# Optimization experiments

Hardware: AMD Instinct MI355X
Metric: run time of the kernel (lower is better)

The kernel has to match this reference:

```python
import jax, jax.numpy as jnp
import numpy as np

B, NPER, K = 32, 256, 32
N, E = B * NPER, B * NPER * 32
H, NF, NG, L = 128, 128, 50, 6
CUTOFF = 10.0
LOG2 = 0.6931471805599453


def _ssp(x):
    # ShiftedSoftplus: softplus(x) - log(2)
    return jax.nn.softplus(x) - LOG2


def setup_inputs() -> dict:
    key = jax.random.key(0)
    ks = jax.random.split(key, 16)
    rng = np.random.default_rng(0)

    pos = jnp.asarray(rng.uniform(0.0, 5.0, size=(N, 3)).astype(np.float32))
    z = jnp.asarray(rng.integers(1, 100, size=(N,)).astype(np.int32))
    batch = jnp.asarray((np.arange(N) // NPER).astype(np.int32))
    # K neighbors per atom, within the same graph, no self-loops; dst sorted
    dst = np.repeat(np.arange(N), K)
    off = rng.integers(1, NPER, size=N * K)
    src = (dst % NPER + off) % NPER + (dst // NPER) * NPER
    edge_index = jnp.asarray(np.stack([src, dst]).astype(np.int32))
    domain_ids = jnp.asarray(rng.integers(0, 5, size=(B,)).astype(np.int32))

    def dense(k, i, o):
        return jax.random.normal(k, (i, o), jnp.float32) / np.sqrt(i)

    def stackw(k, i, o):
        return jax.random.normal(k, (L, i, o), jnp.float32) / np.sqrt(i)

    return {
        'pos': pos, 'z': z, 'batch': batch, 'edge_index': edge_index,
        'domain_ids': domain_ids,
        'embedding': jax.random.normal(ks[0], (100, H), jnp.float32),
        'mlp_w1': stackw(ks[1], NG, NF), 'mlp_b1': jnp.zeros((L, NF), jnp.float32),
        'mlp_w2': stackw(ks[2], NF, NF), 'mlp_b2': jnp.zeros((L, NF), jnp.float32),
        'cf_lin1_w': stackw(ks[3], H, NF),
        'cf_lin2_w': stackw(ks[4], NF, H), 'cf_lin2_b': jnp.zeros((L, H), jnp.float32),
        'int_lin_w': stackw(ks[5], H, H), 'int_lin_b': jnp.zeros((L, H), jnp.float32),
        'out_w1': dense(ks[6], H, H // 2), 'out_b1': jnp.zeros((H // 2,), jnp.float32),
        'out_w2': dense(ks[7], H // 2, 1), 'out_b2': jnp.zeros((1,), jnp.float32),
        'dom_emb': jax.random.normal(ks[8], (5, 64), jnp.float32),
        'film_w1': dense(ks[9], 64, 128), 'film_b1': jnp.zeros((128,), jnp.float32),
        'film_w2': dense(ks[10], 128, 128), 'film_b2': jnp.zeros((128,), jnp.float32),
        'gamma_w': dense(ks[11], 128, H), 'gamma_b': jnp.zeros((H,), jnp.float32),
        'beta_w': dense(ks[12], 128, H), 'beta_b': jnp.zeros((H,), jnp.float32),
    }


def reference(pos, z, batch, edge_index, domain_ids, embedding,
              mlp_w1, mlp_b1, mlp_w2, mlp_b2, cf_lin1_w, cf_lin2_w, cf_lin2_b,
              int_lin_w, int_lin_b, out_w1, out_b1, out_w2, out_b2,
              dom_emb, film_w1, film_b1, film_w2, film_b2,
              gamma_w, gamma_b, beta_w, beta_b):
    n_atoms = pos.shape[0]
    n_graphs = domain_ids.shape[0]
    src, dst = edge_index[0], edge_index[1]

    # edge distances, gaussian smearing, cosine cutoff (computed once)
    d = jnp.sqrt(jnp.sum((pos[src] - pos[dst]) ** 2, axis=-1))          # [E]
    offsets = jnp.linspace(0.0, CUTOFF, NG).astype(pos.dtype)
    coeff = -0.5 / (CUTOFF / (NG - 1)) ** 2
    edge_attr = jnp.exp(coeff * (d[:, None] - offsets) ** 2)            # [E,NG]
    C = 0.5 * (jnp.cos(d * (np.pi / CUTOFF)) + 1.0)                     # [E]

    h = embedding[z]                                                    # [N,H]
    for l in range(L):
        # filter network on gaussian basis, modulated by cosine cutoff
        W = (_ssp(edge_attr @ mlp_w1[l] + mlp_b1[l]) @ mlp_w2[l] + mlp_b2[l]) * C[:, None]  # [E,NF]
        x = h @ cf_lin1_w[l]                                            # [N,NF]
        msg = x[src] * W                                                # [E,NF]
        agg = jax.ops.segment_sum(msg, dst, num_segments=n_atoms)       # [N,NF]
        x = agg @ cf_lin2_w[l] + cf_lin2_b[l]                           # [N,H]
        h = h + _ssp(x) @ int_lin_w[l] + int_lin_b[l]                   # residual

    atom_e = _ssp(h @ out_w1 + out_b1) @ out_w2 + out_b2                # [N,1]
    e_graph = jax.ops.segment_sum(atom_e, batch, num_segments=n_graphs) # [B,1]

    # FiLM domain bias (features are zeros, so gamma path contributes 0 - faithful)
    de = dom_emb[domain_ids]                                            # [B,64]
    film = jax.nn.relu(de @ film_w1 + film_b1) @ film_w2 + film_b2      # [B,128]
    gamma = film @ gamma_w + gamma_b                                    # [B,H]
    beta = film @ beta_w + beta_b                                       # [B,H]
    dummy = jnp.zeros((n_graphs, H), pos.dtype)
    bias = jnp.sum(gamma * dummy + beta, axis=-1)                       # [B]

    # faithful broadcast [B,1]+[B] -> [B,B], then sum(dim=1) as in original
    energy = jnp.sum(e_graph + bias[None, :], axis=1)                   # [B]

    forces = jnp.zeros((n_atoms, 3), energy.dtype)
    stress = jnp.zeros((n_graphs, 3, 3), energy.dtype)
    features = jnp.zeros((n_atoms, H), energy.dtype)
    return energy, forces, stress, features
```

## Files before the change

kernel.cpp:

```cpp
#include <hip/hip_runtime.h>
#include <math.h>

using uint = unsigned int;
typedef _Float16 h2    __attribute__((ext_vector_type(2)));
typedef _Float16 f16x8 __attribute__((ext_vector_type(8)));
typedef float    f32x4 __attribute__((ext_vector_type(4)));

#define N_ATOMS 8192
#define NEDGE   262144
#define KNBR    32
#define NGAUSS  50
#define NLAYER  6
#define NB      32
#define GTAB    1024
#define DMAX    8.6603f
#define FCUT    10.0f
#define MB      1048576

#define LSTRIDE 76
#define S_WT    0
#define S_AS    9728
#define S_TS    10944
#define GEMM_SMEM 12160

#define T_W1    0
#define T_W2    4096
#define T_RBF   12288
#define T_HID   13312
#define TAB_SMEM 15360

#define OW1P_OFF 147456
#define M1_OFF   151552
#define M2_OFF   176128
#define WPACK_N  225280

__device__ __forceinline__ float ssp(float x) {
    return fmaxf(x, 0.0f) + log1pf(expf(-fabsf(x))) - 0.69314718055994531f;
}
__device__ __forceinline__ uint pack2(float a, float b) {
    union { h2 h; uint u; } x;
    h2 v; v.x = (_Float16)a; v.y = (_Float16)b; x.h = v; return x.u;
}
__device__ __forceinline__ h2 u2h(uint u) {
    union { uint u; h2 h; } x; x.u = u; return x.h;
}
__device__ __forceinline__ uint h2u(h2 h) {
    union { h2 h; uint u; } x; x.h = h; return x.u;
}
__device__ __forceinline__ float fdot2f(h2 a, h2 b, float c) {
#if __has_builtin(__builtin_amdgcn_fdot2)
    return __builtin_amdgcn_fdot2(a, b, c, false);
#else
    return fmaf((float)a.y, (float)b.y, fmaf((float)a.x, (float)b.x, c));
#endif
}

__device__ __forceinline__ void stage_cp(uint* sm, const uint* __restrict__ src,
                                         int n16, int tid) {
    for (int i = tid; i < n16; i += 256) {
        uint4 v = ((const uint4*)src)[i];
        *(uint4*)&sm[(i >> 4) * LSTRIDE + (i & 15) * 4] = v;
    }
}

template<int NCT>
__device__ __forceinline__ void run_gemm(const uint* sm, int as_off, int lane,
                                         int nb, f32x4* acc) {
    int m = lane & 15, q = lane >> 4;
    #pragma unroll
    for (int ks = 0; ks < 4; ++ks) {
        f16x8 a = *(const f16x8*)&sm[as_off + m * LSTRIDE + q * 4 + ks * 16];
        #pragma unroll
        for (int ct = 0; ct < NCT; ++ct) {
            f16x8 b = *(const f16x8*)&sm[S_WT + (nb + ct * 16 + m) * LSTRIDE + q * 4 + ks * 16];
            acc[ct] = __builtin_amdgcn_mfma_f32_16x16x32_f16(a, b, acc[ct], 0, 0, 0);
        }
    }
}

struct SArgs {
    const float *pos; const int *z; const int *ei; const int *dom;
    const float *emb;
    const float *cf1; const float *cf2w; const float *intw; const float *ow1;
    const float *mw1; const float *mw2;
    const float *dome; const float *fw1; const float *fb1;
    const float *fw2; const float *fb2; const float *bw; const float *bb;
    uint2 *epack; float *h; uint *xA;
    float *gbias; uint *wpack; float *out; int out_size;
};

__global__ void __launch_bounds__(256) k_setup(SArgs a) {
    __shared__ __align__(16) uint sm[S_AS + 1216];
    const int tid = threadIdx.x, bid = blockIdx.x;
    const int gidx = bid * 256 + tid, gsz = 512 * 256;
    const int lane = tid & 63, w = tid >> 6;
    const int m = lane & 15, q = lane >> 4;
    const int rowbase = bid * 16;

    for (int i = gidx; i < a.out_size; i += gsz) a.out[i] = 0.0f;

    for (int idx = gidx; idx < WPACK_N; idx += gsz) {
        if (idx < OW1P_OFF) {
            int mat = idx >> 13, e = idx & 8191;
            int kp = e >> 7, c = e & 127;
            const float* src = (mat < 6) ? (a.cf1 + mat * 16384)
                            : (mat < 12) ? (a.cf2w + (mat - 6) * 16384)
                                         : (a.intw + (mat - 12) * 16384);
            a.wpack[mat * 8192 + c * 64 + kp] =
                pack2(src[2 * kp * 128 + c], src[(2 * kp + 1) * 128 + c]);
        } else if (idx < M1_OFF) {
            int e = idx - OW1P_OFF;
            int kp = e >> 6, c = e & 63;
            a.wpack[OW1P_OFF + c * 64 + kp] =
                pack2(a.ow1[2 * kp * 64 + c], a.ow1[(2 * kp + 1) * 64 + c]);
        } else if (idx < M2_OFF) {
            int e = idx - M1_OFF;
            int l = e >> 12, r = e & 4095;
            int kp = r >> 7, c = r & 127;
            int g0 = 2 * kp;
            float va = (g0 < NGAUSS)     ? a.mw1[l*NGAUSS*128 + g0*128 + c]     : 0.f;
            float vb = (g0 + 1 < NGAUSS) ? a.mw1[l*NGAUSS*128 + (g0+1)*128 + c] : 0.f;
            a.wpack[idx] = pack2(va, vb);
        } else {
            int e = idx - M2_OFF;
            int l = e >> 13, r = e & 8191;
            int kp = r >> 7, c = r & 127;
            a.wpack[idx] = pack2(a.mw2[l*16384 + 2*kp*128 + c],
                                 a.mw2[l*16384 + (2*kp+1)*128 + c]);
        }
    }

    const float invdelta = (float)(GTAB - 1) / DMAX;
    #pragma unroll
    for (int t = 0; t < 2; ++t) {
        int e = rowbase * KNBR + t * 256 + tid;
        int s = a.ei[e], d = a.ei[NEDGE + e];
        float dx = a.pos[3*s] - a.pos[3*d];
        float dy = a.pos[3*s+1] - a.pos[3*d+1];
        float dz = a.pos[3*s+2] - a.pos[3*d+2];
        float dist = sqrtf(dx*dx + dy*dy + dz*dz);
        float u = dist * invdelta;
        int i0 = (int)u; i0 = (i0 < GTAB - 2) ? i0 : (GTAB - 2);
        float t2 = u - (float)i0;
        uint tb = pack2(t2, 0.0f) & 0xffffu;
        uint2 ep; ep.x = (uint)s; ep.y = (tb << 16) | (uint)i0;
        a.epack[e] = ep;
    }

    for (int i = tid; i < 1024; i += 256) {
        int r = i >> 6, f2 = i & 63;
        int zz = a.z[rowbase + r];
        float2 v = *(const float2*)&a.emb[zz * 128 + f2 * 2];
        *(float2*)&a.h[(rowbase + r) * 128 + f2 * 2] = v;
        sm[S_AS + r * LSTRIDE + f2] = pack2(v.x, v.y);
    }
    for (int i = tid; i < 2048; i += 256) {
        int m4 = i >> 7, c = i & 127;
        float v[8];
        #pragma unroll
        for (int j = 0; j < 8; ++j) v[j] = a.cf1[(8 * m4 + j) * 128 + c];
        uint4 pk; pk.x = pack2(v[0], v[1]); pk.y = pack2(v[2], v[3]);
        pk.z = pack2(v[4], v[5]); pk.w = pack2(v[6], v[7]);
        *(uint4*)&sm[c * LSTRIDE + m4 * 4] = pk;
    }
    __syncthreads();
    {
        f32x4 acc[2] = {{0,0,0,0},{0,0,0,0}};
        run_gemm<2>(sm, S_AS, lane, w * 32, acc);
        #pragma unroll
        for (int ct = 0; ct < 2; ++ct) {
            int n = w * 32 + ct * 16 + m;
            #pragma unroll
            for (int i = 0; i < 4; ++i) {
                float v = acc[ct][i];
                float u = __shfl_xor(v, 1, 64);
                if (!(lane & 1))
                    a.xA[(rowbase + q * 4 + i) * 64 + (n >> 1)] = pack2(v, u);
            }
        }
    }
    __syncthreads();
    if (bid >= 32 && bid < 64) {
        int g = bid - 32;
        float* fs = (float*)sm;
        if (tid < 64) fs[tid] = a.dome[a.dom[g] * 64 + tid];
        __syncthreads();
        if (tid < 128) {
            float acc = a.fb1[tid];
            for (int i = 0; i < 64; ++i) acc = fmaf(fs[i], a.fw1[i*128 + tid], acc);
            fs[64 + tid] = fmaxf(acc, 0.0f);
        }
        __syncthreads();
        if (tid < 128) {
            float acc = a.fb2[tid];
            for (int i = 0; i < 128; ++i) acc = fmaf(fs[64+i], a.fw2[i*128 + tid], acc);
            fs[192 + tid] = acc;
        }
        __syncthreads();
        if (tid < 128) {
            float acc = a.bb[tid];
            for (int i = 0; i < 128; ++i) acc = fmaf(fs[192+i], a.bw[i*128 + tid], acc);
            #pragma unroll
            for (int off = 32; off > 0; off >>= 1) acc += __shfl_down(acc, off, 64);
            if ((tid & 63) == 0) fs[320 + (tid >> 6)] = acc;
        }
        __syncthreads();
        if (tid == 0) a.gbias[g] = fs[320] + fs[321];
    }
}

__global__ void __launch_bounds__(256) k_table(
    const uint* __restrict__ wpack, const float* __restrict__ mb1,
    const float* __restrict__ mb2, uint* __restrict__ tab) {
    __shared__ __align__(16) uint sm[TAB_SMEM];
    const int tid = threadIdx.x;
    const int l = blockIdx.x >> 5;
    const int base = (blockIdx.x & 31) * 32;
    { const uint4* s4 = (const uint4*)(wpack + M1_OFF + l*4096);
      uint4* d4 = (uint4*)&sm[T_W1];
      for (int i = tid; i < 1024; i += 256) d4[i] = s4[i]; }
    { const uint4* s4 = (const uint4*)(wpack + M2_OFF + l*8192);
      uint4* d4 = (uint4*)&sm[T_W2];
      for (int i = tid; i < 2048; i += 256) d4[i] = s4[i]; }
    const float delta = DMAX / (float)(GTAB - 1);
    const float gstep = FCUT / (float)(NGAUSS - 1);
    const float coeff = -0.5f / (gstep * gstep);
    for (int i = tid; i < 1024; i += 256) {
        int r = i >> 5, kp = i & 31;
        float dv = (float)(base + r) * delta;
        int g0 = 2 * kp;
        float v0 = 0.f, v1 = 0.f;
        if (g0 < NGAUSS)     { float t = dv - (float)g0 * gstep;     v0 = expf(coeff*t*t); }
        if (g0 + 1 < NGAUSS) { float t = dv - (float)(g0+1) * gstep; v1 = expf(coeff*t*t); }
        sm[T_RBF + i] = pack2(v0, v1);
    }
    __syncthreads();
    int tx = tid & 31, ty = tid >> 5, c0 = tx * 4, tr0 = ty * 4;
    float acc[4][4];
    #pragma unroll
    for (int i = 0; i < 4; ++i) { acc[i][0]=0.f; acc[i][1]=0.f; acc[i][2]=0.f; acc[i][3]=0.f; }
    #pragma unroll
    for (int oct = 0; oct < 8; ++oct) {
        int kp0 = oct * 4;
        uint4 w_[4];
        #pragma unroll
        for (int p = 0; p < 4; ++p) w_[p] = *(const uint4*)&sm[T_W1 + (kp0+p)*128 + c0];
        #pragma unroll
        for (int i = 0; i < 4; ++i) {
            uint4 av = *(const uint4*)&sm[T_RBF + (tr0+i)*32 + kp0];
            uint aa[4] = {av.x, av.y, av.z, av.w};
            #pragma unroll
            for (int p = 0; p < 4; ++p) {
                h2 ap = u2h(aa[p]);
                acc[i][0] = fdot2f(ap, u2h(w_[p].x), acc[i][0]);
                acc[i][1] = fdot2f(ap, u2h(w_[p].y), acc[i][1]);
                acc[i][2] = fdot2f(ap, u2h(w_[p].z), acc[i][2]);
                acc[i][3] = fdot2f(ap, u2h(w_[p].w), acc[i][3]);
            }
        }
    }
    float4 b1v = *(const float4*)&mb1[l*128 + c0];
    #pragma unroll
    for (int i = 0; i < 4; ++i) {
        uint2 o;
        o.x = pack2(ssp(acc[i][0] + b1v.x), ssp(acc[i][1] + b1v.y));
        o.y = pack2(ssp(acc[i][2] + b1v.z), ssp(acc[i][3] + b1v.w));
        *(uint2*)&sm[T_HID + (tr0+i)*64 + (c0 >> 1)] = o;
    }
    __syncthreads();
    float acc2[4][4];
    #pragma unroll
    for (int i = 0; i < 4; ++i) { acc2[i][0]=0.f; acc2[i][1]=0.f; acc2[i][2]=0.f; acc2[i][3]=0.f; }
    #pragma unroll 4
    for (int oct = 0; oct < 16; ++oct) {
        int kp0 = oct * 4;
        uint4 w_[4];
        #pragma unroll
        for (int p = 0; p < 4; ++p) w_[p] = *(const uint4*)&sm[T_W2 + (kp0+p)*128 + c0];
        #pragma unroll
        for (int i = 0; i < 4; ++i) {
            uint4 av = *(const uint4*)&sm[T_HID + (tr0+i)*64 + kp0];
            uint aa[4] = {av.x, av.y, av.z, av.w};
            #pragma unroll
            for (int p = 0; p < 4; ++p) {
                h2 ap = u2h(aa[p]);
                acc2[i][0] = fdot2f(ap, u2h(w_[p].x), acc2[i][0]);
                acc2[i][1] = fdot2f(ap, u2h(w_[p].y), acc2[i][1]);
                acc2[i][2] = fdot2f(ap, u2h(w_[p].z), acc2[i][2]);
                acc2[i][3] = fdot2f(ap, u2h(w_[p].w), acc2[i][3]);
            }
        }
    }
    float4 b2v = *(const float4*)&mb2[l*128 + c0];
    #pragma unroll
    for (int i = 0; i < 4; ++i) {
        int row = base + tr0 + i;
        float dv = (float)row * delta;
        float Cd = 0.5f * (cosf(dv * 0.3141592653589793f) + 1.0f);
        uint2 o;
        o.x = pack2((acc2[i][0] + b2v.x)*Cd, (acc2[i][1] + b2v.y)*Cd);
        o.y = pack2((acc2[i][2] + b2v.z)*Cd, (acc2[i][3] + b2v.w)*Cd);
        *(uint2*)&tab[(l*GTAB + row)*64 + (c0 >> 1)] = o;
    }
}

__global__ void __launch_bounds__(256) k_gather(
    const uint* __restrict__ xin, const uint* __restrict__ tabl,
    const uint2* __restrict__ epack, uint* __restrict__ agg) {
    const int tid = threadIdx.x;
    const int lane = tid & 63;
    const int atom = blockIdx.x * 4 + (tid >> 6);
    const int ebase = atom * KNBR;
    uint2 ep = epack[ebase + (lane & 31)];
    uint sv = ep.x, yv = ep.y;
    h2 acc; acc.x = (_Float16)0; acc.y = (_Float16)0;
    #pragma unroll 8
    for (int k = 0; k < KNBR; ++k) {
        uint s = __shfl(sv, k, 64);
        uint y = __shfl(yv, k, 64);
        int i0 = (int)(y & 0xffffu);
        uint th = y >> 16;
        h2 t2 = u2h(th | (th << 16));
        h2 f0 = u2h(tabl[i0 * 64 + lane]);
        h2 f1 = u2h(tabl[(i0 + 1) * 64 + lane]);
        h2 xs = u2h(xin[s * 64 + lane]);
        h2 wv = f0 + t2 * (f1 - f0);
        acc = acc + xs * wv;
    }
    agg[atom * 64 + lane] = h2u(acc);
}

template<bool LAST>
__global__ void __launch_bounds__(256) k_gemmL(
    float* __restrict__ h, const uint* __restrict__ agg, uint* __restrict__ xout,
    const uint* __restrict__ w2p, const uint* __restrict__ w3p,
    const uint* __restrict__ w1np,
    const float* __restrict__ b2, const float* __restrict__ b3,
    const float* __restrict__ ob1, const float* __restrict__ ow2,
    const float* __restrict__ ob2, const float* __restrict__ gbias,
    float* __restrict__ out) {
    __shared__ __align__(16) uint sm[GEMM_SMEM];
    const int tid = threadIdx.x, bid = blockIdx.x;
    const int lane = tid & 63, w = tid >> 6;
    const int m = lane & 15, q = lane >> 4;
    const int rowbase = bid * 16;

    stage_cp(sm, w2p, 2048, tid);
    {
        const uint4* a4 = (const uint4*)(agg + rowbase * 64);
        for (int i = tid; i < 256; i += 256) {
            uint4 v = a4[i];
            *(uint4*)&sm[S_AS + (i >> 4) * LSTRIDE + (i & 15) * 4] = v;
        }
    }
    __syncthreads();
    {
        f32x4 acc[2] = {{0,0,0,0},{0,0,0,0}};
        run_gemm<2>(sm, S_AS, lane, w * 32, acc);
        #pragma unroll
        for (int ct = 0; ct < 2; ++ct) {
            int n = w * 32 + ct * 16 + m;
            float bv = b2[n];
            #pragma unroll
            for (int i = 0; i < 4; ++i) {
                float v = ssp(acc[ct][i] + bv);
                float u = __shfl_xor(v, 1, 64);
                if (!(lane & 1))
                    sm[S_TS + (q * 4 + i) * LSTRIDE + (n >> 1)] = pack2(v, u);
            }
        }
    }
    __syncthreads();
    stage_cp(sm, w3p, 2048, tid);
    __syncthreads();
    {
        f32x4 acc[2] = {{0,0,0,0},{0,0,0,0}};
        run_gemm<2>(sm, S_TS, lane, w * 32, acc);
        #pragma unroll
        for (int ct = 0; ct < 2; ++ct) {
            int n = w * 32 + ct * 16 + m;
            float bv = b3[n];
            #pragma unroll
            for (int i = 0; i < 4; ++i) {
                int r = rowbase + q * 4 + i;
                float hv = h[r * 128 + n] + acc[ct][i] + bv;
                h[r * 128 + n] = hv;
                float u = __shfl_xor(hv, 1, 64);
                if (!(lane & 1))
                    sm[S_AS + (q * 4 + i) * LSTRIDE + (n >> 1)] = pack2(hv, u);
            }
        }
    }
    __syncthreads();
    if (!LAST) {
        stage_cp(sm, w1np, 2048, tid);
        __syncthreads();
        f32x4 acc[2] = {{0,0,0,0},{0,0,0,0}};
        run_gemm<2>(sm, S_AS, lane, w * 32, acc);
        #pragma unroll
        for (int ct = 0; ct < 2; ++ct) {
            int n = w * 32 + ct * 16 + m;
            #pragma unroll
            for (int i = 0; i < 4; ++i) {
                float v = acc[ct][i];
                float u = __shfl_xor(v, 1, 64);
                if (!(lane & 1))
                    xout[(rowbase + q * 4 + i) * 64 + (n >> 1)] = pack2(v, u);
            }
        }
    } else {
        stage_cp(sm, w1np, 1024, tid);
        __syncthreads();
        f32x4 acc[1] = {{0,0,0,0}};
        run_gemm<1>(sm, S_AS, lane, w * 16, acc);
        int n = w * 16 + m;
        float b1v = ob1[n], w2v = ow2[n];
        float part = 0.f;
        #pragma unroll
        for (int i = 0; i < 4; ++i) part += ssp(acc[0][i] + b1v) * w2v;
        #pragma unroll
        for (int mm = 1; mm < 64; mm <<= 1) part += __shfl_xor(part, mm, 64);
        float* fs = (float*)&sm[S_TS];
        if (lane == 0) fs[w] = part;
        __syncthreads();
        if (tid == 0) {
            float bsum = fs[0] + fs[1] + fs[2] + fs[3] + 16.0f * ob2[0];
            float add = 32.0f * bsum;
            if ((bid & 15) == 0) {
                float sb = 0.f;
                for (int j = 0; j < NB; ++j) sb += gbias[j];
                add += sb;
            }
            atomicAdd(&out[bid >> 4], add);
        }
    }
}

extern "C" void kernel_launch(void* const* d_in, const int* in_sizes, int n_in,
                              void* d_out, int out_size, void* d_ws, size_t ws_size,
                              hipStream_t stream) {
    SArgs a;
    a.pos  = (const float*)d_in[0];
    a.z    = (const int*)d_in[1];
    a.ei   = (const int*)d_in[3];
    a.dom  = (const int*)d_in[4];
    a.emb  = (const float*)d_in[5];
    a.mw1  = (const float*)d_in[6];
    const float* mb1 = (const float*)d_in[7];
    a.mw2  = (const float*)d_in[8];
    const float* mb2 = (const float*)d_in[9];
    a.cf1  = (const float*)d_in[10];
    a.cf2w = (const float*)d_in[11];
    const float* cf2b = (const float*)d_in[12];
    a.intw = (const float*)d_in[13];
    const float* intb = (const float*)d_in[14];
    a.ow1  = (const float*)d_in[15];
    const float* ob1  = (const float*)d_in[16];
    const float* ow2  = (const float*)d_in[17];
    const float* ob2  = (const float*)d_in[18];
    a.dome = (const float*)d_in[19];
    a.fw1  = (const float*)d_in[20];
    a.fb1  = (const float*)d_in[21];
    a.fw2  = (const float*)d_in[22];
    a.fb2  = (const float*)d_in[23];
    a.bw   = (const float*)d_in[26];
    a.bb   = (const float*)d_in[27];

    char* ws = (char*)d_ws;
    a.epack   = (uint2*)(ws + 0);
    uint* tab = (uint*)(ws + 2*MB);
    a.h       = (float*)(ws + 4*MB);
    a.xA      = (uint*)(ws + 8*MB);
    uint* xB  = (uint*)(ws + 10*MB);
    uint* agg = (uint*)(ws + 12*MB);
    a.gbias   = (float*)(ws + 14*MB);
    a.wpack   = (uint*)(ws + 14*MB + 4096);
    a.out = (float*)d_out;
    a.out_size = out_size;

    k_setup<<<512, 256, 0, stream>>>(a);
    k_table<<<192, 256, 0, stream>>>(a.wpack, mb1, mb2, tab);

    const uint* xr = a.xA;
    uint* xw = xB;
    for (int l = 0; l < NLAYER; ++l) {
        k_gather<<<N_ATOMS/4, 256, 0, stream>>>(xr, tab + l*GTAB*64, a.epack, agg);
        const uint* w2p = a.wpack + (6 + l) * 8192;
        const uint* w3p = a.wpack + (12 + l) * 8192;
        if (l < NLAYER - 1) {
            k_gemmL<false><<<512, 256, 0, stream>>>(
                a.h, agg, xw, w2p, w3p, a.wpack + (l + 1) * 8192,
                cf2b + l*128, intb + l*128, ob1, ow2, ob2, a.gbias, a.out);
        } else {
            k_gemmL<true><<<512, 256, 0, stream>>>(
                a.h, agg, xw, w2p, w3p, a.wpack + OW1P_OFF,
                cf2b + l*128, intb + l*128, ob1, ow2, ob2, a.gbias, a.out);
        }
        const uint* tmp = xr; xr = xw; xw = (uint*)tmp;
    }
}
```

Before: 273.2 us.

## Fuse filter-table build into setup, interleave table rows, prefetch GEMM weights to registers

The filter-table kernel is merged into k_setup as extra blocks, with MLP weight packing done directly in shared memory, which removes one launch. The table layout now stores each row together with the next row's values, so the gather does one 16-byte load per edge instead of two separate row loads. The gather also splits the 32 edges across two half-waves, each lane handling 4 features, and adds the halves with a cross-lane shuffle. The layer GEMM kernel prefetches the w3/w1 weights and h values into registers at kernel start to hide global latency, at the cost of more registers and a doubled table size.

```diff
diff --git a/kernel.cpp b/kernel.cpp
--- a/kernel.cpp
+++ b/kernel.cpp
@@ -21,18 +21,14 @@
 #define S_WT    0
 #define S_AS    9728
 #define S_TS    10944
-#define GEMM_SMEM 12160
-
 #define T_W1    0
 #define T_W2    4096
 #define T_RBF   12288
 #define T_HID   13312
-#define TAB_SMEM 15360
+#define SMEM_N  15616
 
 #define OW1P_OFF 147456
-#define M1_OFF   151552
-#define M2_OFF   176128
-#define WPACK_N  225280
+#define WPACK_N  151552
 
 __device__ __forceinline__ float ssp(float x) {
     return fmaxf(x, 0.0f) + log1pf(expf(-fabsf(x))) - 0.69314718055994531f;
@@ -82,19 +78,121 @@
     const float *pos; const int *z; const int *ei; const int *dom;
     const float *emb;
     const float *cf1; const float *cf2w; const float *intw; const float *ow1;
-    const float *mw1; const float *mw2;
+    const float *mw1; const float *mb1; const float *mw2; const float *mb2;
     const float *dome; const float *fw1; const float *fb1;
     const float *fw2; const float *fb2; const float *bw; const float *bb;
-    uint2 *epack; float *h; uint *xA;
+    uint2 *epack; uint *tab2; float *h; uint *xA;
     float *gbias; uint *wpack; float *out; int out_size;
 };
 
 __global__ void __launch_bounds__(256) k_setup(SArgs a) {
-    __shared__ __align__(16) uint sm[S_AS + 1216];
+    __shared__ __align__(16) uint sm[SMEM_N];
     const int tid = threadIdx.x, bid = blockIdx.x;
-    const int gidx = bid * 256 + tid, gsz = 512 * 256;
     const int lane = tid & 63, w = tid >> 6;
     const int m = lane & 15, q = lane >> 4;
+
+    if (bid >= 512) {
+        int c = bid - 512;
+        int l = c >> 5;
+        int base = (c & 31) * 32;
+        for (int i = tid; i < 4096; i += 256) {
+            int kp = i >> 7, cc = i & 127;
+            int g0 = 2 * kp;
+            float va = (g0 < NGAUSS)     ? a.mw1[l*NGAUSS*128 + g0*128 + cc]     : 0.f;
+            float vb = (g0 + 1 < NGAUSS) ? a.mw1[l*NGAUSS*128 + (g0+1)*128 + cc] : 0.f;
+            sm[T_W1 + i] = pack2(va, vb);
+        }
+        for (int i = tid; i < 8192; i += 256) {
+            int kp = i >> 7, cc = i & 127;
+            sm[T_W2 + i] = pack2(a.mw2[l*16384 + 2*kp*128 + cc],
+                                 a.mw2[l*16384 + (2*kp+1)*128 + cc]);
+        }
+        const float delta = DMAX / (float)(GTAB - 1);
+        const float gstep = FCUT / (float)(NGAUSS - 1);
+        const float coeff = -0.5f / (gstep * gstep);
+        for (int i = tid; i < 1024; i += 256) {
+            int r = i >> 5, kp = i & 31;
+            float dv = (float)(base + r) * delta;
+            int g0 = 2 * kp;
+            float v0 = 0.f, v1 = 0.f;
+            if (g0 < NGAUSS)     { float t = dv - (float)g0 * gstep;     v0 = expf(coeff*t*t); }
+            if (g0 + 1 < NGAUSS) { float t = dv - (float)(g0+1) * gstep; v1 = expf(coeff*t*t); }
+            sm[T_RBF + i] = pack2(v0, v1);
+        }
+        __syncthreads();
+        int tx = tid & 31, ty = tid >> 5, c0 = tx * 4, tr0 = ty * 4;
+        float acc[4][4];
+        #pragma unroll
+        for (int i = 0; i < 4; ++i) { acc[i][0]=0.f; acc[i][1]=0.f; acc[i][2]=0.f; acc[i][3]=0.f; }
+        #pragma unroll
+        for (int oct = 0; oct < 8; ++oct) {
+            int kp0 = oct * 4;
+            uint4 w_[4];
+            #pragma unroll
+            for (int p = 0; p < 4; ++p) w_[p] = *(const uint4*)&sm[T_W1 + (kp0+p)*128 + c0];
+            #pragma unroll
+            for (int i = 0; i < 4; ++i) {
+                uint4 av = *(const uint4*)&sm[T_RBF + (tr0+i)*32 + kp0];
+                uint aa[4] = {av.x, av.y, av.z, av.w};
+                #pragma unroll
+                for (int p = 0; p < 4; ++p) {
+                    h2 ap = u2h(aa[p]);
+                    acc[i][0] = fdot2f(ap, u2h(w_[p].x), acc[i][0]);
+                    acc[i][1] = fdot2f(ap, u2h(w_[p].y), acc[i][1]);
+                    acc[i][2] = fdot2f(ap, u2h(w_[p].z), acc[i][2]);
+                    acc[i][3] = fdot2f(ap, u2h(w_[p].w), acc[i][3]);
+                }
+            }
+        }
+        float4 b1v = *(const float4*)&a.mb1[l*128 + c0];
+        #pragma unroll
+        for (int i = 0; i < 4; ++i) {
+            uint2 o;
+            o.x = pack2(ssp(acc[i][0] + b1v.x), ssp(acc[i][1] + b1v.y));
+            o.y = pack2(ssp(acc[i][2] + b1v.z), ssp(acc[i][3] + b1v.w));
+            *(uint2*)&sm[T_HID + (tr0+i)*64 + (c0 >> 1)] = o;
+        }
+        __syncthreads();
+        float acc2[4][4];
+        #pragma unroll
+        for (int i = 0; i < 4; ++i) { acc2[i][0]=0.f; acc2[i][1]=0.f; acc2[i][2]=0.f; acc2[i][3]=0.f; }
+        #pragma unroll 4
+        for (int oct = 0; oct < 16; ++oct) {
+            int kp0 = oct * 4;
+            uint4 w_[4];
+            #pragma unroll
+            for (int p = 0; p < 4; ++p) w_[p] = *(const uint4*)&sm[T_W2 + (kp0+p)*128 + c0];
+            #pragma unroll
+            for (int i = 0; i < 4; ++i) {
+                uint4 av = *(const uint4*)&sm[T_HID + (tr0+i)*64 + kp0];
+                uint aa[4] = {av.x, av.y, av.z, av.w};
+                #pragma unroll
+                for (int p = 0; p < 4; ++p) {
+                    h2 ap = u2h(aa[p]);
+                    acc2[i][0] = fdot2f(ap, u2h(w_[p].x), acc2[i][0]);
+                    acc2[i][1] = fdot2f(ap, u2h(w_[p].y), acc2[i][1]);
+                    acc2[i][2] = fdot2f(ap, u2h(w_[p].z), acc2[i][2]);
+                    acc2[i][3] = fdot2f(ap, u2h(w_[p].w), acc2[i][3]);
+                }
+            }
+        }
+        float4 b2v = *(const float4*)&a.mb2[l*128 + c0];
+        #pragma unroll
+        for (int i = 0; i < 4; ++i) {
+            int row = base + tr0 + i;
+            float dv = (float)row * delta;
+            float Cd = 0.5f * (cosf(dv * 0.3141592653589793f) + 1.0f);
+            uint2 o;
+            o.x = pack2((acc2[i][0] + b2v.x)*Cd, (acc2[i][1] + b2v.y)*Cd);
+            o.y = pack2((acc2[i][2] + b2v.z)*Cd, (acc2[i][3] + b2v.w)*Cd);
+            *(uint2*)&a.tab2[(l*GTAB + row)*128 + tx*4] = o;
+            if (row > 0)
+                *(uint2*)&a.tab2[(l*GTAB + row - 1)*128 + tx*4 + 2] = o;
+        }
+        return;
+    }
+
+    const int gidx = bid * 256 + tid, gsz = 512 * 256;
     const int rowbase = bid * 16;
 
     for (int i = gidx; i < a.out_size; i += gsz) a.out[i] = 0.0f;
@@ -102,31 +200,17 @@
     for (int idx = gidx; idx < WPACK_N; idx += gsz) {
         if (idx < OW1P_OFF) {
             int mat = idx >> 13, e = idx & 8191;
-            int kp = e >> 7, c = e & 127;
+            int kp = e >> 7, cc = e & 127;
             const float* src = (mat < 6) ? (a.cf1 + mat * 16384)
                             : (mat < 12) ? (a.cf2w + (mat - 6) * 16384)
                                          : (a.intw + (mat - 12) * 16384);
-            a.wpack[mat * 8192 + c * 64 + kp] =
-                pack2(src[2 * kp * 128 + c], src[(2 * kp + 1) * 128 + c]);
-        } else if (idx < M1_OFF) {
+            a.wpack[mat * 8192 + cc * 64 + kp] =
+                pack2(src[2 * kp * 128 + cc], src[(2 * kp + 1) * 128 + cc]);
+        } else {
             int e = idx - OW1P_OFF;
-            int kp = e >> 6, c = e & 63;
-            a.wpack[OW1P_OFF + c * 64 + kp] =
-                pack2(a.ow1[2 * kp * 64 + c], a.ow1[(2 * kp + 1) * 64 + c]);
-        } else if (idx < M2_OFF) {
-            int e = idx - M1_OFF;
-            int l = e >> 12, r = e & 4095;
-            int kp = r >> 7, c = r & 127;
-            int g0 = 2 * kp;
-            float va = (g0 < NGAUSS)     ? a.mw1[l*NGAUSS*128 + g0*128 + c]     : 0.f;
-            float vb = (g0 + 1 < NGAUSS) ? a.mw1[l*NGAUSS*128 + (g0+1)*128 + c] : 0.f;
-            a.wpack[idx] = pack2(va, vb);
-        } else {
-            int e = idx - M2_OFF;
-            int l = e >> 13, r = e & 8191;
-            int kp = r >> 7, c = r & 127;
-            a.wpack[idx] = pack2(a.mw2[l*16384 + 2*kp*128 + c],
-                                 a.mw2[l*16384 + (2*kp+1)*128 + c]);
+            int kp = e >> 6, cc = e & 63;
+            a.wpack[OW1P_OFF + cc * 64 + kp] =
+                pack2(a.ow1[2 * kp * 64 + cc], a.ow1[(2 * kp + 1) * 64 + cc]);
         }
     }
 
@@ -155,13 +239,13 @@
         sm[S_AS + r * LSTRIDE + f2] = pack2(v.x, v.y);
     }
     for (int i = tid; i < 2048; i += 256) {
-        int m4 = i >> 7, c = i & 127;
+        int m4 = i >> 7, cc = i & 127;
         float v[8];
         #pragma unroll
-        for (int j = 0; j < 8; ++j) v[j] = a.cf1[(8 * m4 + j) * 128 + c];
+        for (int j = 0; j < 8; ++j) v[j] = a.cf1[(8 * m4 + j) * 128 + cc];
         uint4 pk; pk.x = pack2(v[0], v[1]); pk.y = pack2(v[2], v[3]);
         pk.z = pack2(v[4], v[5]); pk.w = pack2(v[6], v[7]);
-        *(uint4*)&sm[c * LSTRIDE + m4 * 4] = pk;
+        *(uint4*)&sm[cc * LSTRIDE + m4 * 4] = pk;
     }
     __syncthreads();
     {
@@ -209,125 +293,38 @@
     }
 }
 
-__global__ void __launch_bounds__(256) k_table(
-    const uint* __restrict__ wpack, const float* __restrict__ mb1,
-    const float* __restrict__ mb2, uint* __restrict__ tab) {
-    __shared__ __align__(16) uint sm[TAB_SMEM];
-    const int tid = threadIdx.x;
-    const int l = blockIdx.x >> 5;
-    const int base = (blockIdx.x & 31) * 32;
-    { const uint4* s4 = (const uint4*)(wpack + M1_OFF + l*4096);
-      uint4* d4 = (uint4*)&sm[T_W1];
-      for (int i = tid; i < 1024; i += 256) d4[i] = s4[i]; }
-    { const uint4* s4 = (const uint4*)(wpack + M2_OFF + l*8192);
-      uint4* d4 = (uint4*)&sm[T_W2];
-      for (int i = tid; i < 2048; i += 256) d4[i] = s4[i]; }
-    const float delta = DMAX / (float)(GTAB - 1);
-    const float gstep = FCUT / (float)(NGAUSS - 1);
-    const float coeff = -0.5f / (gstep * gstep);
-    for (int i = tid; i < 1024; i += 256) {
-        int r = i >> 5, kp = i & 31;
-        float dv = (float)(base + r) * delta;
-        int g0 = 2 * kp;
-        float v0 = 0.f, v1 = 0.f;
-        if (g0 < NGAUSS)     { float t = dv - (float)g0 * gstep;     v0 = expf(coeff*t*t); }
-        if (g0 + 1 < NGAUSS) { float t = dv - (float)(g0+1) * gstep; v1 = expf(coeff*t*t); }
-        sm[T_RBF + i] = pack2(v0, v1);
-    }
-    __syncthreads();
-    int tx = tid & 31, ty = tid >> 5, c0 = tx * 4, tr0 = ty * 4;
-    float acc[4][4];
-    #pragma unroll
-    for (int i = 0; i < 4; ++i) { acc[i][0]=0.f; acc[i][1]=0.f; acc[i][2]=0.f; acc[i][3]=0.f; }
-    #pragma unroll
-    for (int oct = 0; oct < 8; ++oct) {
-        int kp0 = oct * 4;
-        uint4 w_[4];
-        #pragma unroll
-        for (int p = 0; p < 4; ++p) w_[p] = *(const uint4*)&sm[T_W1 + (kp0+p)*128 + c0];
-        #pragma unroll
-        for (int i = 0; i < 4; ++i) {
-            uint4 av = *(const uint4*)&sm[T_RBF + (tr0+i)*32 + kp0];
-            uint aa[4] = {av.x, av.y, av.z, av.w};
-            #pragma unroll
-            for (int p = 0; p < 4; ++p) {
-                h2 ap = u2h(aa[p]);
-                acc[i][0] = fdot2f(ap, u2h(w_[p].x), acc[i][0]);
-                acc[i][1] = fdot2f(ap, u2h(w_[p].y), acc[i][1]);
-                acc[i][2] = fdot2f(ap, u2h(w_[p].z), acc[i][2]);
-                acc[i][3] = fdot2f(ap, u2h(w_[p].w), acc[i][3]);
-            }
-        }
-    }
-    float4 b1v = *(const float4*)&mb1[l*128 + c0];
-    #pragma unroll
-    for (int i = 0; i < 4; ++i) {
-        uint2 o;
-        o.x = pack2(ssp(acc[i][0] + b1v.x), ssp(acc[i][1] + b1v.y));
-        o.y = pack2(ssp(acc[i][2] + b1v.z), ssp(acc[i][3] + b1v.w));
-        *(uint2*)&sm[T_HID + (tr0+i)*64 + (c0 >> 1)] = o;
-    }
-    __syncthreads();
-    float acc2[4][4];
-    #pragma unroll
-    for (int i = 0; i < 4; ++i) { acc2[i][0]=0.f; acc2[i][1]=0.f; acc2[i][2]=0.f; acc2[i][3]=0.f; }
-    #pragma unroll 4
-    for (int oct = 0; oct < 16; ++oct) {
-        int kp0 = oct * 4;
-        uint4 w_[4];
-        #pragma unroll
-        for (int p = 0; p < 4; ++p) w_[p] = *(const uint4*)&sm[T_W2 + (kp0+p)*128 + c0];
-        #pragma unroll
-        for (int i = 0; i < 4; ++i) {
-            uint4 av = *(const uint4*)&sm[T_HID + (tr0+i)*64 + kp0];
-            uint aa[4] = {av.x, av.y, av.z, av.w};
-            #pragma unroll
-            for (int p = 0; p < 4; ++p) {
-                h2 ap = u2h(aa[p]);
-                acc2[i][0] = fdot2f(ap, u2h(w_[p].x), acc2[i][0]);
-                acc2[i][1] = fdot2f(ap, u2h(w_[p].y), acc2[i][1]);
-                acc2[i][2] = fdot2f(ap, u2h(w_[p].z), acc2[i][2]);
-                acc2[i][3] = fdot2f(ap, u2h(w_[p].w), acc2[i][3]);
-            }
-        }
-    }
-    float4 b2v = *(const float4*)&mb2[l*128 + c0];
-    #pragma unroll
-    for (int i = 0; i < 4; ++i) {
-        int row = base + tr0 + i;
-        float dv = (float)row * delta;
-        float Cd = 0.5f * (cosf(dv * 0.3141592653589793f) + 1.0f);
-        uint2 o;
-        o.x = pack2((acc2[i][0] + b2v.x)*Cd, (acc2[i][1] + b2v.y)*Cd);
-        o.y = pack2((acc2[i][2] + b2v.z)*Cd, (acc2[i][3] + b2v.w)*Cd);
-        *(uint2*)&tab[(l*GTAB + row)*64 + (c0 >> 1)] = o;
-    }
-}
-
 __global__ void __launch_bounds__(256) k_gather(
-    const uint* __restrict__ xin, const uint* __restrict__ tabl,
+    const uint* __restrict__ xin, const uint* __restrict__ tab2l,
     const uint2* __restrict__ epack, uint* __restrict__ agg) {
     const int tid = threadIdx.x;
     const int lane = tid & 63;
     const int atom = blockIdx.x * 4 + (tid >> 6);
-    const int ebase = atom * KNBR;
-    uint2 ep = epack[ebase + (lane & 31)];
-    uint sv = ep.x, yv = ep.y;
-    h2 acc; acc.x = (_Float16)0; acc.y = (_Float16)0;
-    #pragma unroll 8
-    for (int k = 0; k < KNBR; ++k) {
-        uint s = __shfl(sv, k, 64);
-        uint y = __shfl(yv, k, 64);
+    const int side = lane >> 5, l5 = lane & 31;
+    uint2 ep = epack[atom * KNBR + l5];
+    h2 a0; a0.x = (_Float16)0; a0.y = (_Float16)0;
+    h2 a1 = a0;
+    #pragma unroll 4
+    for (int k = 0; k < 16; ++k) {
+        int e = 2 * k + side;
+        uint s = __shfl(ep.x, e, 64);
+        uint y = __shfl(ep.y, e, 64);
         int i0 = (int)(y & 0xffffu);
         uint th = y >> 16;
         h2 t2 = u2h(th | (th << 16));
-        h2 f0 = u2h(tabl[i0 * 64 + lane]);
-        h2 f1 = u2h(tabl[(i0 + 1) * 64 + lane]);
-        h2 xs = u2h(xin[s * 64 + lane]);
-        h2 wv = f0 + t2 * (f1 - f0);
-        acc = acc + xs * wv;
-    }
-    agg[atom * 64 + lane] = h2u(acc);
+        uint4 tv = *(const uint4*)&tab2l[i0 * 128 + l5 * 4];
+        uint2 xv = *(const uint2*)&xin[s * 64 + l5 * 2];
+        h2 w0 = u2h(tv.x) + t2 * (u2h(tv.z) - u2h(tv.x));
+        h2 w1 = u2h(tv.y) + t2 * (u2h(tv.w) - u2h(tv.y));
+        a0 = a0 + u2h(xv.x) * w0;
+        a1 = a1 + u2h(xv.y) * w1;
+    }
+    uint u0 = h2u(a0), u1 = h2u(a1);
+    uint p0 = __shfl_xor(u0, 32, 64), p1 = __shfl_xor(u1, 32, 64);
+    if (side == 0) {
+        h2 r0 = u2h(u0) + u2h(p0), r1 = u2h(u1) + u2h(p1);
+        uint2 o; o.x = h2u(r0); o.y = h2u(r1);
+        *(uint2*)&agg[atom * 64 + l5 * 2] = o;
+    }
 }
 
 template<bool LAST>
@@ -339,20 +336,27 @@
     const float* __restrict__ ob1, const float* __restrict__ ow2,
     const float* __restrict__ ob2, const float* __restrict__ gbias,
     float* __restrict__ out) {
-    __shared__ __align__(16) uint sm[GEMM_SMEM];
+    __shared__ __align__(16) uint sm[S_TS + 1216];
     const int tid = threadIdx.x, bid = blockIdx.x;
     const int lane = tid & 63, w = tid >> 6;
     const int m = lane & 15, q = lane >> 4;
     const int rowbase = bid * 16;
 
+    constexpr int NW1 = LAST ? 4 : 8;
+    uint4 w3r[8], w1r[NW1];
+    #pragma unroll
+    for (int j = 0; j < 8; ++j) w3r[j] = ((const uint4*)w3p)[tid + 256 * j];
+    #pragma unroll
+    for (int j = 0; j < NW1; ++j) w1r[j] = ((const uint4*)w1np)[tid + 256 * j];
+    float hr[2][4];
+    #pragma unroll
+    for (int ct = 0; ct < 2; ++ct)
+        #pragma unroll
+        for (int i = 0; i < 4; ++i)
+            hr[ct][i] = h[(rowbase + q * 4 + i) * 128 + w * 32 + ct * 16 + m];
     stage_cp(sm, w2p, 2048, tid);
-    {
-        const uint4* a4 = (const uint4*)(agg + rowbase * 64);
-        for (int i = tid; i < 256; i += 256) {
-            uint4 v = a4[i];
-            *(uint4*)&sm[S_AS + (i >> 4) * LSTRIDE + (i & 15) * 4] = v;
-        }
-    }
+    {   uint4 v = ((const uint4*)(agg + rowbase * 64))[tid];
+        *(uint4*)&sm[S_AS + (tid >> 4) * LSTRIDE + (tid & 15) * 4] = v; }
     __syncthreads();
     {
         f32x4 acc[2] = {{0,0,0,0},{0,0,0,0}};
@@ -371,7 +375,11 @@
         }
     }
     __syncthreads();
-    stage_cp(sm, w3p, 2048, tid);
+    #pragma unroll
+    for (int j = 0; j < 8; ++j) {
+        int i = tid + 256 * j;
+        *(uint4*)&sm[(i >> 4) * LSTRIDE + (i & 15) * 4] = w3r[j];
+    }
     __syncthreads();
     {
         f32x4 acc[2] = {{0,0,0,0},{0,0,0,0}};
@@ -383,7 +391,7 @@
             #pragma unroll
             for (int i = 0; i < 4; ++i) {
                 int r = rowbase + q * 4 + i;
-                float hv = h[r * 128 + n] + acc[ct][i] + bv;
+                float hv = hr[ct][i] + acc[ct][i] + bv;
                 h[r * 128 + n] = hv;
                 float u = __shfl_xor(hv, 1, 64);
                 if (!(lane & 1))
@@ -392,9 +400,13 @@
         }
     }
     __syncthreads();
+    #pragma unroll
+    for (int j = 0; j < NW1; ++j) {
+        int i = tid + 256 * j;
+        *(uint4*)&sm[(i >> 4) * LSTRIDE + (i & 15) * 4] = w1r[j];
+    }
+    __syncthreads();
     if (!LAST) {
-        stage_cp(sm, w1np, 2048, tid);
-        __syncthreads();
         f32x4 acc[2] = {{0,0,0,0},{0,0,0,0}};
         run_gemm<2>(sm, S_AS, lane, w * 32, acc);
         #pragma unroll
@@ -409,8 +421,6 @@
             }
         }
     } else {
-        stage_cp(sm, w1np, 1024, tid);
-        __syncthreads();
         f32x4 acc[1] = {{0,0,0,0}};
         run_gemm<1>(sm, S_AS, lane, w * 16, acc);
         int n = w * 16 + m;
@@ -446,9 +456,9 @@
     a.dom  = (const int*)d_in[4];
     a.emb  = (const float*)d_in[5];
     a.mw1  = (const float*)d_in[6];
-    const float* mb1 = (const float*)d_in[7];
+    a.mb1  = (const float*)d_in[7];
     a.mw2  = (const float*)d_in[8];
-    const float* mb2 = (const float*)d_in[9];
+    a.mb2  = (const float*)d_in[9];
     a.cf1  = (const float*)d_in[10];
     a.cf2w = (const float*)d_in[11];
     const float* cf2b = (const float*)d_in[12];
@@ -467,24 +477,23 @@
     a.bb   = (const float*)d_in[27];
 
     char* ws = (char*)d_ws;
-    a.epack   = (uint2*)(ws + 0);
-    uint* tab = (uint*)(ws + 2*MB);
-    a.h       = (float*)(ws + 4*MB);
-    a.xA      = (uint*)(ws + 8*MB);
-    uint* xB  = (uint*)(ws + 10*MB);
-    uint* agg = (uint*)(ws + 12*MB);
-    a.gbias   = (float*)(ws + 14*MB);
-    a.wpack   = (uint*)(ws + 14*MB + 4096);
+    a.epack  = (uint2*)(ws + 0);
+    a.tab2   = (uint*)(ws + 2*MB);
+    a.h      = (float*)(ws + 5*MB);
+    a.xA     = (uint*)(ws + 9*MB);
+    uint* xB = (uint*)(ws + 11*MB);
+    uint* agg= (uint*)(ws + 13*MB);
+    a.gbias  = (float*)(ws + 15*MB);
+    a.wpack  = (uint*)(ws + 15*MB + 4096);
     a.out = (float*)d_out;
     a.out_size = out_size;
 
-    k_setup<<<512, 256, 0, stream>>>(a);
-    k_table<<<192, 256, 0, stream>>>(a.wpack, mb1, mb2, tab);
+    k_setup<<<704, 256, 0, stream>>>(a);
 
     const uint* xr = a.xA;
     uint* xw = xB;
     for (int l = 0; l < NLAYER; ++l) {
-        k_gather<<<N_ATOMS/4, 256, 0, stream>>>(xr, tab + l*GTAB*64, a.epack, agg);
+        k_gather<<<N_ATOMS/4, 256, 0, stream>>>(xr, a.tab2 + l*GTAB*128, a.epack, agg);
         const uint* w2p = a.wpack + (6 + l) * 8192;
         const uint* w3p = a.wpack + (12 + l) * 8192;
         if (l < NLAYER - 1) {
```

New measurement: 321.8 us. 1.18x slower.
